# Kernel optimization log

Measured on AMD Instinct MI355X. Metric: run time of the kernel, lower is better.

## Reference

```python
import jax, jax.numpy as jnp
import numpy as np

T, B, H = 400, 256, 256
XE, SE, NX, NS = 32, 16, 100, 5
DIN = XE + H + 1  # x_emb + f_old(hidden) + treatment scalar


def _gru(x, h, wih, whh, bih, bhh):
    # torch.nn.GRUCell math, gate order r,z,n
    gx = x @ wih + bih
    gh = h @ whh + bhh
    xr, xz, xn = jnp.split(gx, 3, axis=-1)
    hr, hz, hn = jnp.split(gh, 3, axis=-1)
    r = jax.nn.sigmoid(xr + hr)
    z = jax.nn.sigmoid(xz + hz)
    n = jnp.tanh(xn + r * hn)
    return (1.0 - z) * n + z * h


def setup_inputs():
    key = jax.random.key(0)
    ks = iter(jax.random.split(key, 64))
    rn = lambda shape, s=0.05: jax.random.normal(next(ks), shape, jnp.float32) * s
    z = lambda n: jnp.zeros((n,), jnp.float32)
    return {
        "x": rn((B, T, NX), 1.0),
        "x_demo": rn((B, NS), 1.0),
        "x_fr": (jax.random.uniform(next(ks), (B, T)) < 0.1).astype(jnp.float32),
        "f_hx0": rn((B, H), 1.0),
        "cf_hx0": rn((B, H), 1.0),
        "w_x2emb": rn((NX, XE)), "b_x2emb": z(XE),
        "w_static": rn((NS, SE)), "b_static": z(SE),
        "wih_f": rn((DIN, 3 * H)), "whh_f": rn((H, 3 * H)), "bih_f": z(3 * H), "bhh_f": z(3 * H),
        "wih_cf": rn((DIN, 3 * H)), "whh_cf": rn((H, 3 * H)), "bih_cf": z(3 * H), "bhh_cf": z(3 * H),
        "w_cat_f": rn((2 * H, H)), "b_cat_f": z(H),
        "w_cat_cf": rn((2 * H, H)), "b_cat_cf": z(H),
        "w_ipw": rn((XE + H + SE, H)), "b_ipw": z(H), "w_ipw_out": rn((H, 1)),
        "w_of": rn((XE + H + SE + 1, H)), "b_of": z(H), "w_ho_f": rn((H, 1)),
        "w_ocf": rn((XE + H + SE + 1, H)), "b_ocf": z(H), "w_ho_cf": rn((H, 1)),
    }


def _forward(x, x_demo, x_fr, f_hx0, cf_hx0,
             w_x2emb, b_x2emb, w_static, b_static,
             wih_f, whh_f, bih_f, bhh_f,
             wih_cf, whh_cf, bih_cf, bhh_cf,
             w_cat_f, b_cat_f, w_cat_cf, b_cat_cf,
             w_ipw, b_ipw, w_ipw_out,
             w_of, b_of, w_ho_f,
             w_ocf, b_ocf, w_ho_cf):
    x_emb_all = jnp.einsum('btf,fe->tbe', x, w_x2emb) + b_x2emb  # (T,B,XE)
    cf_tr = (x_fr.sum(1) == 0).astype(x.dtype)[:, None]          # (B,1), constant over steps
    tidx = jnp.arange(T)

    def attn_ctx(h, buf, i):
        # 'dot' attention of current hidden vs previous hiddens (positions < i)
        scores = jnp.sum(h[None, :, :] * buf, axis=-1)            # (T,B)
        scores = jnp.where((tidx < i)[:, None], scores, -1e30)
        w = jax.nn.softmax(scores, axis=0)
        return jnp.einsum('tb,tbh->bh', w, buf)                   # (B,H)

    def step(carry, xs):
        i, f_hx, cf_hx, f_old, cf_old, f_buf, cf_buf = carry
        x_emb, fr_t = xs
        f_zx = jnp.concatenate([x_emb, f_old], -1)                # (B,XE+H)
        cf_zx = jnp.concatenate([x_emb, cf_old], -1)
        f_hx = _gru(jnp.concatenate([f_zx, fr_t[:, None]], -1), f_hx, wih_f, whh_f, bih_f, bhh_f)
        cf_hx = _gru(jnp.concatenate([cf_zx, cf_tr], -1), cf_hx, wih_cf, whh_cf, bih_cf, bhh_cf)
        # i == 0: torch concatenates (f_hx, f_hx); otherwise attention context
        f_ctx = jnp.where(i == 0, f_hx, attn_ctx(f_hx, f_buf, i))
        cf_ctx = jnp.where(i == 0, cf_hx, attn_ctx(cf_hx, cf_buf, i))
        f_old = jnp.tanh(jnp.concatenate([f_hx, f_ctx], -1) @ w_cat_f + b_cat_f)
        cf_old = jnp.tanh(jnp.concatenate([cf_hx, cf_ctx], -1) @ w_cat_cf + b_cat_cf)
        f_buf = f_buf.at[i].set(f_hx)
        cf_buf = cf_buf.at[i].set(cf_hx)
        return (i + 1, f_hx, cf_hx, f_old, cf_old, f_buf, cf_buf), (f_zx, cf_zx)

    init = (jnp.int32(0), f_hx0, cf_hx0, f_hx0, cf_hx0,
            jnp.zeros((T, B, H), x.dtype), jnp.zeros((T, B, H), x.dtype))
    _, (f_zxs, cf_zxs) = jax.lax.scan(step, init, (x_emb_all, x_fr.T))  # (T,B,XE+H)

    demo = x_demo @ w_static + b_static                            # (B,SE)
    demo_b = jnp.broadcast_to(demo, (T, B, SE))
    ipw = jax.nn.relu(jnp.concatenate([f_zxs, demo_b], -1) @ w_ipw + b_ipw) @ w_ipw_out  # (T,B,1)
    f_tr = (x_fr.sum(1) > 0).astype(x.dtype)[:, None]
    f_h = jax.nn.relu(jnp.concatenate([f_zxs.max(0), demo, f_tr], -1) @ w_of + b_of)
    f_out = f_h @ w_ho_f
    cf_h = jax.nn.relu(jnp.concatenate([cf_zxs.max(0), demo, 1.0 - f_tr], -1) @ w_ocf + b_ocf)
    cf_out = cf_h @ w_ho_cf
    return ipw, f_out, cf_out, f_h


def reference(x, x_demo, x_fr, f_hx0, cf_hx0,
              w_x2emb, b_x2emb, w_static, b_static,
              wih_f, whh_f, bih_f, bhh_f,
              wih_cf, whh_cf, bih_cf, bhh_cf,
              w_cat_f, b_cat_f, w_cat_cf, b_cat_cf,
              w_ipw, b_ipw, w_ipw_out,
              w_of, b_of, w_ho_f,
              w_ocf, b_ocf, w_ho_cf):
    return _forward(x, x_demo, x_fr, f_hx0, cf_hx0,
                    w_x2emb, b_x2emb, w_static, b_static,
                    wih_f, whh_f, bih_f, bhh_f,
                    wih_cf, whh_cf, bih_cf, bhh_cf,
                    w_cat_f, b_cat_f, w_cat_cf, b_cat_cf,
                    w_ipw, b_ipw, w_ipw_out,
                    w_of, b_of, w_ho_f,
                    w_ocf, b_ocf, w_ho_cf)
```

## Files before the change

### kernel.cpp

```cpp
#include <hip/hip_runtime.h>


#define TT 400
#define BB 256
#define HH 256
#define XEc 32
#define NXc 100
#define SEc 16
#define G3 768
#define KXc 289

constexpr size_t XEMB_O     = 0;
constexpr size_t FBUF_O     = XEMB_O     + (size_t)TT*BB*XEc;
constexpr size_t CFBUF_O    = FBUF_O     + (size_t)BB*TT*HH;
constexpr size_t FHX_O      = CFBUF_O    + (size_t)BB*TT*HH;
constexpr size_t CFHX_O     = FHX_O      + (size_t)2*BB*HH;
constexpr size_t FOLD_O     = CFHX_O     + (size_t)2*BB*HH;
constexpr size_t CFOLD_O    = FOLD_O     + (size_t)2*BB*HH;
constexpr size_t CTXF_O     = CFOLD_O    + (size_t)2*BB*HH;
constexpr size_t CTXCF_O    = CTXF_O     + (size_t)BB*HH;
constexpr size_t DEMO_O     = CTXCF_O    + (size_t)BB*HH;
constexpr size_t DEMOIPW_O  = DEMO_O     + (size_t)BB*SEc;
constexpr size_t TRF_O      = DEMOIPW_O  + (size_t)BB*HH;
constexpr size_t XEMBMAX_O  = TRF_O      + (size_t)BB;
constexpr size_t FOLDMAX_O  = XEMBMAX_O  + (size_t)BB*XEc;
constexpr size_t CFOLDMAX_O = FOLDMAX_O  + (size_t)BB*HH;
constexpr size_t BAR_O      = CFOLDMAX_O + (size_t)BB*HH;
constexpr int    BAR_WORDS  = 4096;

constexpr size_t IPW_OUT   = 0;
constexpr size_t FOUT_OUT  = 102400;
constexpr size_t CFOUT_OUT = 102656;
constexpr size_t FH_OUT    = 102912;

struct P {
  const float *x, *x_demo, *x_fr, *f_hx0, *cf_hx0;
  const float *w_x2emb, *b_x2emb, *w_static, *b_static;
  const float *wih_f, *whh_f, *bih_f, *bhh_f;
  const float *wih_cf, *whh_cf, *bih_cf, *bhh_cf;
  const float *w_cat_f, *b_cat_f, *w_cat_cf, *b_cat_cf;
  const float *w_ipw, *b_ipw, *w_ipw_out;
  const float *w_of, *b_of, *w_ho_f;
  const float *w_ocf, *b_ocf, *w_ho_cf;
  float *out; float *ws;
};

__device__ __forceinline__ float sigm(float v) { return 1.f / (1.f + expf(-v)); }

__device__ __forceinline__ void gsyncg(float* ws, int wg, unsigned target) {
  __syncthreads();
  unsigned* flags = reinterpret_cast<unsigned*>(ws + BAR_O);
  const int tid = threadIdx.x;
  if (tid == 0)
    __hip_atomic_store(&flags[wg * 16], target, __ATOMIC_RELEASE, __HIP_MEMORY_SCOPE_AGENT);
  const int gbase = (wg & ~15) * 16;
  if (tid < 16) {
    while (__hip_atomic_load(&flags[gbase + tid * 16], __ATOMIC_ACQUIRE,
                             __HIP_MEMORY_SCOPE_AGENT) < target)
      __builtin_amdgcn_s_sleep(1);
  }
  __syncthreads();
}

__global__ __launch_bounds__(256) void preA_k(P p) {
  __shared__ float wle[NXc * XEc];
  __shared__ float xt[64 * NXc];
  float* ws = p.ws;
  const int t = blockIdx.x;
  for (int i = threadIdx.x; i < NXc * XEc; i += 256) wle[i] = p.w_x2emb[i];
  const int e = threadIdx.x & 31, r0 = threadIdx.x >> 5;
  for (int bt = 0; bt < 4; ++bt) {
    __syncthreads();
    for (int i = threadIdx.x; i < 64 * NXc; i += 256) {
      int r = i / NXc, f = i - r * NXc;
      xt[i] = p.x[((size_t)(bt * 64 + r) * TT + t) * NXc + f];
    }
    __syncthreads();
    for (int r = r0; r < 64; r += 8) {
      const float* xr = xt + r * NXc;
      float acc = p.b_x2emb[e];
      for (int f = 0; f < NXc; ++f) acc += xr[f] * wle[f * XEc + e];
      ws[XEMB_O + ((size_t)t * BB + bt * 64 + r) * XEc + e] = acc;
    }
  }
}

__global__ __launch_bounds__(256) void preB_k(P p) {
  float* ws = p.ws;
  const int tid = threadIdx.x;
  const int blk = blockIdx.x;
  if (blk < 32) {
    int g = blk * 256 + tid;
    int b = g >> 5, e = g & 31;
    float m = -3.4e38f;
    for (int t = 0; t < TT; ++t)
      m = fmaxf(m, ws[XEMB_O + ((size_t)t * BB + b) * XEc + e]);
    ws[XEMBMAX_O + g] = m;
  } else if (blk < 64) {
    int g = (blk - 32) * 256 + tid;
    for (size_t i = g; i < 102912; i += 8192) p.out[i] = 0.f;
  } else if (blk == 64) {
    for (int i = tid; i < BB * SEc; i += 256) {
      int b = i >> 4, se = i & 15;
      float acc = p.b_static[se];
      for (int ns = 0; ns < 5; ++ns) acc += p.x_demo[b * 5 + ns] * p.w_static[ns * SEc + se];
      ws[DEMO_O + i] = acc;
    }
  } else if (blk < 81) {
    int g = (blk - 65) * 256 + tid;
    for (int i = g; i < BB * HH; i += 4096) {
      int b = i >> 8, j = i & 255;
      float acc = 0.f;
      for (int se = 0; se < SEc; ++se) {
        float d = p.b_static[se];
        for (int ns = 0; ns < 5; ++ns) d += p.x_demo[b * 5 + ns] * p.w_static[ns * SEc + se];
        acc += d * p.w_ipw[(size_t)(288 + se) * HH + j];
      }
      ws[DEMOIPW_O + i] = acc;
    }
  } else if (blk == 81) {
    int b = tid;
    float s = 0.f;
    for (int t = 0; t < TT; ++t) s += p.x_fr[(size_t)b * TT + t];
    ws[TRF_O + b] = (s > 0.f) ? 1.f : 0.f;
  } else if (blk < 98) {
    int g = (blk - 82) * 256 + tid;
    for (int i = g; i < 6 * BB * HH; i += 4096) {
      int a = i >> 16, r = i & 65535;
      float vf = p.f_hx0[r], vc = p.cf_hx0[r];
      size_t off; float v;
      switch (a) {
        case 0: off = FHX_O;      v = vf; break;
        case 1: off = CFHX_O;     v = vc; break;
        case 2: off = FOLD_O;     v = vf; break;
        case 3: off = CFOLD_O;    v = vc; break;
        case 4: off = FOLDMAX_O;  v = vf; break;
        default: off = CFOLDMAX_O; v = vc; break;
      }
      ws[off + r] = v;
    }
  } else if (blk == 98) {
    unsigned* bw = reinterpret_cast<unsigned*>(ws + BAR_O);
    for (int i = tid; i < BAR_WORDS; i += 256) bw[i] = 0u;
  }
}

__global__ __launch_bounds__(1024) void seq_k(P p) {
  __shared__ float lds[13344];
  float* ws = p.ws;
  const int tid = threadIdx.x;
  const int wg = blockIdx.x;
  const int btile = wg >> 4, slice = wg & 15;
  const int cell = slice >> 3, sl = slice & 7;
  const int b0 = btile * 16;
  const int khalf = tid >> 9;
  const int gr = (tid & 511) >> 5;
  const int gc = tid & 31;
  const int jo = sl * 32 + gc;

  unsigned tgt = 1;

  for (int t = 0; t < TT; ++t) {
    const int rd = t & 1, wr = 1 - rd;

    {
      float* ax  = lds;
      float* ah  = lds + 4640;
      float* red = lds + 8752;
      const float* oldv = ws + (cell ? CFOLD_O : FOLD_O) + (size_t)rd * BB * HH;
      const float* hxv  = ws + (cell ? CFHX_O  : FHX_O ) + (size_t)rd * BB * HH;
      float*       hxn  = ws + (cell ? CFHX_O  : FHX_O ) + (size_t)wr * BB * HH;

      for (int i = tid; i < 16 * KXc; i += 1024) {
        int r = i / KXc, k = i - r * KXc; int b = b0 + r; float v;
        if (k < XEc)            v = ws[XEMB_O + ((size_t)t * BB + b) * XEc + k];
        else if (k < XEc + HH)  v = oldv[(size_t)b * HH + (k - XEc)];
        else                    v = cell ? (1.0f - ws[TRF_O + b]) : p.x_fr[(size_t)b * TT + t];
        ax[r * 290 + k] = v;
      }
      for (int i = tid; i < 16 * 256; i += 1024) {
        int r = i >> 8, k = i & 255;
        ah[r * 257 + k] = hxv[(size_t)(b0 + r) * HH + k];
      }
      __syncthreads();

      float g0 = 0.f, g1 = 0.f, g2 = 0.f;
      if (khalf == 0) {
        const float* a  = ax + gr * 290;
        const float* wk = (cell ? p.wih_cf : p.wih_f) + jo;
        #pragma unroll 4
        for (int k = 0; k < KXc; ++k) {
          float av = a[k];
          g0 += av * wk[0]; g1 += av * wk[256]; g2 += av * wk[512];
          wk += G3;
        }
      } else {
        const float* a  = ah + gr * 257;
        const float* wk = (cell ? p.whh_cf : p.whh_f) + jo;
        #pragma unroll 4
        for (int k = 0; k < 256; ++k) {
          float av = a[k];
          g0 += av * wk[0]; g1 += av * wk[256]; g2 += av * wk[512];
          wk += G3;
        }
      }
      if (khalf == 1) {
        float* rp = red + (gr * 32 + gc) * 3;
        rp[0] = g0; rp[1] = g1; rp[2] = g2;
      }
      __syncthreads();
      if (khalf == 0) {
        const float* bih = cell ? p.bih_cf : p.bih_f;
        const float* bhh = cell ? p.bhh_cf : p.bhh_f;
        const float* rp = red + (gr * 32 + gc) * 3;
        float hr = rp[0], hz = rp[1], hn = rp[2];
        float hprev = ah[gr * 257 + jo];
        float r0 = sigm(g0 + bih[jo]       + hr + bhh[jo]);
        float z0 = sigm(g1 + bih[jo + 256] + hz + bhh[jo + 256]);
        float n0 = tanhf(g2 + bih[jo + 512] + r0 * (hn + bhh[jo + 512]));
        hxn[(size_t)(b0 + gr) * HH + jo] = (1.f - z0) * n0 + z0 * hprev;
      }
    }
    gsyncg(ws, wg, tgt++);

    {
      const int b = wg;
      for (int c = 0; c < 2; ++c) {
        const float* hnew = ws + (c ? CFHX_O : FHX_O) + (size_t)wr * BB * HH + (size_t)b * HH;
        float* buf = ws + (c ? CFBUF_O : FBUF_O) + (size_t)b * TT * HH;
        float* ctx = ws + (c ? CTXCF_O : CTXF_O) + (size_t)b * HH;
        float* q = lds;
        if (tid < 256) { float v = hnew[tid]; q[tid] = v; buf[(size_t)t * HH + tid] = v; }
        __syncthreads();
        if (t == 0) {
          if (tid < 256) ctx[tid] = q[tid];
          __syncthreads();
        } else {
          const int wv = tid >> 6, ln = tid & 63;
          float q0 = q[ln], q1 = q[ln + 64], q2 = q[ln + 128], q3 = q[ln + 192];
          float m = -1e30f, ssum = 0.f, c0 = 0.f, c1 = 0.f, c2 = 0.f, c3 = 0.f;
          int tp = wv;
          for (; tp + 16 < t; tp += 32) {
            const float* ka = buf + (size_t)tp * HH;
            const float* kb = buf + (size_t)(tp + 16) * HH;
            float a0 = ka[ln], a1 = ka[ln + 64], a2 = ka[ln + 128], a3 = ka[ln + 192];
            float e0 = kb[ln], e1 = kb[ln + 64], e2 = kb[ln + 128], e3 = kb[ln + 192];
            float da = a0 * q0 + a1 * q1 + a2 * q2 + a3 * q3;
            float db = e0 * q0 + e1 * q1 + e2 * q2 + e3 * q3;
            #pragma unroll
            for (int off = 32; off; off >>= 1) {
              da += __shfl_xor(da, off, 64);
              db += __shfl_xor(db, off, 64);
            }
            float nm = fmaxf(m, fmaxf(da, db));
            float al = expf(m - nm), pa = expf(da - nm), pb = expf(db - nm);
            ssum = ssum * al + pa + pb;
            c0 = c0 * al + pa * a0 + pb * e0;
            c1 = c1 * al + pa * a1 + pb * e1;
            c2 = c2 * al + pa * a2 + pb * e2;
            c3 = c3 * al + pa * a3 + pb * e3;
            m = nm;
          }
          if (tp < t) {
            const float* kr = buf + (size_t)tp * HH;
            float a0 = kr[ln], a1 = kr[ln + 64], a2 = kr[ln + 128], a3 = kr[ln + 192];
            float d = a0 * q0 + a1 * q1 + a2 * q2 + a3 * q3;
            #pragma unroll
            for (int off = 32; off; off >>= 1) d += __shfl_xor(d, off, 64);
            float nm = fmaxf(m, d);
            float al = expf(m - nm), pv = expf(d - nm);
            ssum = ssum * al + pv;
            c0 = c0 * al + pv * a0; c1 = c1 * al + pv * a1;
            c2 = c2 * al + pv * a2; c3 = c3 * al + pv * a3;
            m = nm;
          }
          float* cm = lds + 256; float* cs = lds + 272; float* cc = lds + 288;
          if (ln == 0) { cm[wv] = m; cs[wv] = ssum; }
          cc[wv * 256 + ln]       = c0;
          cc[wv * 256 + ln + 64]  = c1;
          cc[wv * 256 + ln + 128] = c2;
          cc[wv * 256 + ln + 192] = c3;
          __syncthreads();
          if (tid < 256) {
            float M = cm[0];
            #pragma unroll
            for (int w2 = 1; w2 < 16; ++w2) M = fmaxf(M, cm[w2]);
            float S = 0.f, num = 0.f;
            #pragma unroll
            for (int w2 = 0; w2 < 16; ++w2) {
              float e = expf(cm[w2] - M);
              S   += cs[w2] * e;
              num += cc[w2 * 256 + tid] * e;
            }
            ctx[tid] = num / S;
          }
          __syncthreads();
        }
      }
    }
    gsyncg(ws, wg, tgt++);

    {
      float* ct   = lds;
      float* it   = lds + 8208;
      float* red2 = lds + 12832;
      const float* hnew = ws + (cell ? CFHX_O : FHX_O) + (size_t)wr * BB * HH;
      const float* ctxv = ws + (cell ? CTXCF_O : CTXF_O);
      for (int i = tid; i < 16 * 512; i += 1024) {
        int r = i >> 9, k = i & 511; int b = b0 + r;
        ct[r * 513 + k] = (k < 256) ? hnew[(size_t)b * HH + k]
                                    : ctxv[(size_t)b * HH + (k - 256)];
      }
      for (int i = tid; i < 16 * 288; i += 1024) {
        int r = i / 288, k = i - r * 288; int b = b0 + r;
        it[r * 289 + k] = (k < 32) ? ws[XEMB_O + ((size_t)t * BB + b) * XEc + k]
                                   : ws[FOLD_O + (size_t)rd * BB * HH + (size_t)b * HH + (k - 32)];
      }
      __syncthreads();

      {
        const float* wc = cell ? p.w_cat_cf : p.w_cat_f;
        float a0 = 0.f;
        const float* ar = ct + gr * 513 + khalf * 256;
        const float* wp = wc + (size_t)(khalf * 256) * HH + jo;
        #pragma unroll 4
        for (int k = 0; k < 256; ++k) { a0 += ar[k] * wp[0]; wp += HH; }
        if (khalf == 1) red2[gr * 32 + gc] = a0;
        __syncthreads();
        if (khalf == 0) {
          const float* bc = cell ? p.b_cat_cf : p.b_cat_f;
          float f0 = tanhf(a0 + red2[gr * 32 + gc] + bc[jo]);
          int b = b0 + gr;
          float* on = ws + (cell ? CFOLD_O : FOLD_O) + (size_t)wr * BB * HH;
          on[(size_t)b * HH + jo] = f0;
          if (t < TT - 1) {
            float* fm = ws + (cell ? CFOLDMAX_O : FOLDMAX_O);
            fm[(size_t)b * HH + jo] = fmaxf(fm[(size_t)b * HH + jo], f0);
          }
        }
      }
      {
        const int ir = tid >> 6, il = tid & 63;
        const int itj = il >> 2, ikq = il & 3;
        const int cI = slice * 16 + itj;
        const int b = b0 + ir;
        float acc = 0.f;
        const float* itr = it + ir * 289;
        const float* wi = p.w_ipw + cI;
        #pragma unroll 4
        for (int k = ikq * 72; k < ikq * 72 + 72; ++k) acc += itr[k] * wi[(size_t)k * HH];
        acc += __shfl_xor(acc, 1, 64);
        acc += __shfl_xor(acc, 2, 64);
        float tot = acc + p.b_ipw[cI] + ws[DEMOIPW_O + (size_t)b * HH + cI];
        float pr = (tot > 0.f) ? tot * p.w_ipw_out[cI] : 0.f;
        pr += __shfl_xor(pr, 4, 64);
        pr += __shfl_xor(pr, 8, 64);
        pr += __shfl_xor(pr, 16, 64);
        pr += __shfl_xor(pr, 32, 64);
        if (il == 0) atomicAdd(p.out + IPW_OUT + (size_t)t * BB + b, pr);
      }
    }
    gsyncg(ws, wg, tgt++);
  }
}

__global__ __launch_bounds__(256) void post_k(P p) {
  __shared__ float at[16 * 306];
  float* ws = p.ws;
  const int tid = threadIdx.x;
  const int wg = blockIdx.x;
  const int btile = wg >> 4, slice = wg & 15;
  const int cell = slice >> 3, sl = slice & 7;
  const int b0 = btile * 16;
  const int tb = tid >> 4, tj = tid & 15;

  for (int i = tid; i < 16 * 305; i += 256) {
    int r = i / 305, k = i - r * 305; int b = b0 + r; float v;
    if (k < 32)        v = ws[XEMBMAX_O + (size_t)b * XEc + k];
    else if (k < 288)  v = ws[(cell ? CFOLDMAX_O : FOLDMAX_O) + (size_t)b * HH + (k - 32)];
    else if (k < 304)  v = ws[DEMO_O + (size_t)b * SEc + (k - 288)];
    else { float tr = ws[TRF_O + b]; v = cell ? (1.f - tr) : tr; }
    at[r * 306 + k] = v;
  }
  __syncthreads();

  const int jo = sl * 32 + tj * 2;
  const float* wo  = cell ? p.w_ocf   : p.w_of;
  const float* bo  = cell ? p.b_ocf   : p.b_of;
  const float* who = cell ? p.w_ho_cf : p.w_ho_f;
  float a0 = 0.f, a1 = 0.f;
  const float* ar = at + tb * 306;
  const float* wop = wo + jo;
  for (int k = 0; k < 305; ++k) {
    float a = ar[k];
    float2 w = *(const float2*)(wop + (size_t)k * HH);
    a0 += a * w.x; a1 += a * w.y;
  }
  int b = b0 + tb;
  float h0 = fmaxf(a0 + bo[jo], 0.f), h1 = fmaxf(a1 + bo[jo + 1], 0.f);
  if (!cell) {
    p.out[FH_OUT + (size_t)b * HH + jo]     = h0;
    p.out[FH_OUT + (size_t)b * HH + jo + 1] = h1;
  }
  float pr = h0 * who[jo] + h1 * who[jo + 1];
  pr += __shfl_xor(pr, 8, 16);
  pr += __shfl_xor(pr, 4, 16);
  pr += __shfl_xor(pr, 2, 16);
  pr += __shfl_xor(pr, 1, 16);
  if (tj == 0) atomicAdd(p.out + (cell ? CFOUT_OUT : FOUT_OUT) + b, pr);
}

extern "C" void kernel_launch(void* const* d_in, const int* in_sizes, int n_in,
                              void* d_out, int out_size, void* d_ws, size_t ws_size,
                              hipStream_t stream) {
  (void)in_sizes; (void)n_in; (void)out_size; (void)ws_size;
  P p;
  p.x        = (const float*)d_in[0];
  p.x_demo   = (const float*)d_in[1];
  p.x_fr     = (const float*)d_in[2];
  p.f_hx0    = (const float*)d_in[3];
  p.cf_hx0   = (const float*)d_in[4];
  p.w_x2emb  = (const float*)d_in[5];
  p.b_x2emb  = (const float*)d_in[6];
  p.w_static = (const float*)d_in[7];
  p.b_static = (const float*)d_in[8];
  p.wih_f    = (const float*)d_in[9];
  p.whh_f    = (const float*)d_in[10];
  p.bih_f    = (const float*)d_in[11];
  p.bhh_f    = (const float*)d_in[12];
  p.wih_cf   = (const float*)d_in[13];
  p.whh_cf   = (const float*)d_in[14];
  p.bih_cf   = (const float*)d_in[15];
  p.bhh_cf   = (const float*)d_in[16];
  p.w_cat_f  = (const float*)d_in[17];
  p.b_cat_f  = (const float*)d_in[18];
  p.w_cat_cf = (const float*)d_in[19];
  p.b_cat_cf = (const float*)d_in[20];
  p.w_ipw    = (const float*)d_in[21];
  p.b_ipw    = (const float*)d_in[22];
  p.w_ipw_out= (const float*)d_in[23];
  p.w_of     = (const float*)d_in[24];
  p.b_of     = (const float*)d_in[25];
  p.w_ho_f   = (const float*)d_in[26];
  p.w_ocf    = (const float*)d_in[27];
  p.b_ocf    = (const float*)d_in[28];
  p.w_ho_cf  = (const float*)d_in[29];
  p.out = (float*)d_out;
  p.ws  = (float*)d_ws;

  preA_k<<<dim3(TT), dim3(256), 0, stream>>>(p);
  preB_k<<<dim3(256), dim3(256), 0, stream>>>(p);

  void* kp[] = { &p };
  hipLaunchCooperativeKernel((const void*)seq_k, dim3(256), dim3(1024), kp, 0, stream);

  post_k<<<dim3(256), dim3(256), 0, stream>>>(p);
}
```

Before: 45.92 ms.

## Relax grid-barrier ordering, split GEMV K four ways with paired columns, vectorize attention

The global barrier now uses relaxed agent-scope atomics instead of release/acquire, and polls with a longer sleep. To compensate, every cross-workgroup read and write of shared state goes through relaxed atomic loads and stores. The GRU and cat GEMVs move from a two-way K split with one column per thread to a four-way K split with two adjacent columns per thread. This lets weight loads use float2 and adds a three-way LDS reduction. The attention pass reads keys and the query as float4. The intent is to cut cache-invalidation and barrier overhead and to raise memory-load efficiency. The risks are memory-ordering correctness, since no fences remain, and added wake-up latency from the longer sleep.

Result: slower. 54.69 ms (+19.1%).

```diff
diff --git a/kernel.cpp b/kernel.cpp
--- a/kernel.cpp
+++ b/kernel.cpp
@@ -9,6 +9,9 @@
 #define SEc 16
 #define G3 768
 #define KXc 289
+
+#define AGT __HIP_MEMORY_SCOPE_AGENT
+#define RLX __ATOMIC_RELAXED
 
 constexpr size_t XEMB_O     = 0;
 constexpr size_t FBUF_O     = XEMB_O     + (size_t)TT*BB*XEc;
@@ -47,17 +50,23 @@
 
 __device__ __forceinline__ float sigm(float v) { return 1.f / (1.f + expf(-v)); }
 
+__device__ __forceinline__ float ald(const float* a) {
+  return __hip_atomic_load(a, RLX, AGT);
+}
+__device__ __forceinline__ void ast(float* a, float v) {
+  __hip_atomic_store(a, v, RLX, AGT);
+}
+
 __device__ __forceinline__ void gsyncg(float* ws, int wg, unsigned target) {
   __syncthreads();
   unsigned* flags = reinterpret_cast<unsigned*>(ws + BAR_O);
   const int tid = threadIdx.x;
   if (tid == 0)
-    __hip_atomic_store(&flags[wg * 16], target, __ATOMIC_RELEASE, __HIP_MEMORY_SCOPE_AGENT);
+    __hip_atomic_store(&flags[wg * 16], target, RLX, AGT);
   const int gbase = (wg & ~15) * 16;
   if (tid < 16) {
-    while (__hip_atomic_load(&flags[gbase + tid * 16], __ATOMIC_ACQUIRE,
-                             __HIP_MEMORY_SCOPE_AGENT) < target)
-      __builtin_amdgcn_s_sleep(1);
+    while (__hip_atomic_load(&flags[gbase + tid * 16], RLX, AGT) < target)
+      __builtin_amdgcn_s_sleep(8);
   }
   __syncthreads();
 }
@@ -146,17 +155,17 @@
 }
 
 __global__ __launch_bounds__(1024) void seq_k(P p) {
-  __shared__ float lds[13344];
+  __shared__ float lds[14368];
   float* ws = p.ws;
   const int tid = threadIdx.x;
   const int wg = blockIdx.x;
   const int btile = wg >> 4, slice = wg & 15;
   const int cell = slice >> 3, sl = slice & 7;
   const int b0 = btile * 16;
-  const int khalf = tid >> 9;
-  const int gr = (tid & 511) >> 5;
-  const int gc = tid & 31;
-  const int jo = sl * 32 + gc;
+  const int gcp = tid & 15;
+  const int gr  = (tid >> 4) & 15;
+  const int kq  = tid >> 8;
+  const int jo  = sl * 32 + gcp * 2;
 
   unsigned tgt = 1;
 
@@ -174,51 +183,80 @@
       for (int i = tid; i < 16 * KXc; i += 1024) {
         int r = i / KXc, k = i - r * KXc; int b = b0 + r; float v;
         if (k < XEc)            v = ws[XEMB_O + ((size_t)t * BB + b) * XEc + k];
-        else if (k < XEc + HH)  v = oldv[(size_t)b * HH + (k - XEc)];
+        else if (k < XEc + HH)  v = ald(&oldv[(size_t)b * HH + (k - XEc)]);
         else                    v = cell ? (1.0f - ws[TRF_O + b]) : p.x_fr[(size_t)b * TT + t];
         ax[r * 290 + k] = v;
       }
       for (int i = tid; i < 16 * 256; i += 1024) {
         int r = i >> 8, k = i & 255;
-        ah[r * 257 + k] = hxv[(size_t)(b0 + r) * HH + k];
+        ah[r * 257 + k] = ald(&hxv[(size_t)(b0 + r) * HH + k]);
       }
       __syncthreads();
 
-      float g0 = 0.f, g1 = 0.f, g2 = 0.f;
-      if (khalf == 0) {
+      float g0=0,g1=0,g2=0,g3=0,g4=0,g5=0;
+      if (kq < 2) {
+        const int kbeg = (kq & 1) ? 145 : 0, kend = (kq & 1) ? 289 : 145;
         const float* a  = ax + gr * 290;
-        const float* wk = (cell ? p.wih_cf : p.wih_f) + jo;
-        #pragma unroll 4
-        for (int k = 0; k < KXc; ++k) {
+        const float* wk = (cell ? p.wih_cf : p.wih_f) + (size_t)kbeg * G3 + jo;
+        #pragma unroll 8
+        for (int k = kbeg; k < kend; ++k) {
           float av = a[k];
-          g0 += av * wk[0]; g1 += av * wk[256]; g2 += av * wk[512];
+          float2 w0 = *(const float2*)(wk);
+          float2 w1 = *(const float2*)(wk + 256);
+          float2 w2 = *(const float2*)(wk + 512);
+          g0 += av*w0.x; g1 += av*w0.y;
+          g2 += av*w1.x; g3 += av*w1.y;
+          g4 += av*w2.x; g5 += av*w2.y;
           wk += G3;
         }
       } else {
+        const int kbeg = (kq & 1) ? 128 : 0, kend = kbeg + 128;
         const float* a  = ah + gr * 257;
-        const float* wk = (cell ? p.whh_cf : p.whh_f) + jo;
-        #pragma unroll 4
-        for (int k = 0; k < 256; ++k) {
+        const float* wk = (cell ? p.whh_cf : p.whh_f) + (size_t)kbeg * G3 + jo;
+        #pragma unroll 8
+        for (int k = kbeg; k < kend; ++k) {
           float av = a[k];
-          g0 += av * wk[0]; g1 += av * wk[256]; g2 += av * wk[512];
+          float2 w0 = *(const float2*)(wk);
+          float2 w1 = *(const float2*)(wk + 256);
+          float2 w2 = *(const float2*)(wk + 512);
+          g0 += av*w0.x; g1 += av*w0.y;
+          g2 += av*w1.x; g3 += av*w1.y;
+          g4 += av*w2.x; g5 += av*w2.y;
           wk += G3;
         }
       }
-      if (khalf == 1) {
-        float* rp = red + (gr * 32 + gc) * 3;
-        rp[0] = g0; rp[1] = g1; rp[2] = g2;
+      if (kq != 0) {
+        float* rp = red + (size_t)(kq - 1) * 1536 + (gr * 16 + gcp) * 6;
+        rp[0]=g0; rp[1]=g1; rp[2]=g2; rp[3]=g3; rp[4]=g4; rp[5]=g5;
       }
       __syncthreads();
-      if (khalf == 0) {
+      if (kq == 0) {
         const float* bih = cell ? p.bih_cf : p.bih_f;
         const float* bhh = cell ? p.bhh_cf : p.bhh_f;
-        const float* rp = red + (gr * 32 + gc) * 3;
-        float hr = rp[0], hz = rp[1], hn = rp[2];
-        float hprev = ah[gr * 257 + jo];
-        float r0 = sigm(g0 + bih[jo]       + hr + bhh[jo]);
-        float z0 = sigm(g1 + bih[jo + 256] + hz + bhh[jo + 256]);
-        float n0 = tanhf(g2 + bih[jo + 512] + r0 * (hn + bhh[jo + 512]));
-        hxn[(size_t)(b0 + gr) * HH + jo] = (1.f - z0) * n0 + z0 * hprev;
+        const float* r1 = red +        (gr * 16 + gcp) * 6;
+        const float* r2 = red + 1536 + (gr * 16 + gcp) * 6;
+        const float* r3 = red + 3072 + (gr * 16 + gcp) * 6;
+        int b = b0 + gr;
+        {
+          int j = jo;
+          float xr = g0 + r1[0], xz = g2 + r1[2], xn = g4 + r1[4];
+          float hr = r2[0] + r3[0], hz = r2[2] + r3[2], hn = r2[4] + r3[4];
+          float hprev = ah[gr * 257 + j];
+          float rr = sigm(xr + bih[j]       + hr + bhh[j]);
+          float zz = sigm(xz + bih[j + 256] + hz + bhh[j + 256]);
+          float nn = tanhf(xn + bih[j + 512] + rr * (hn + bhh[j + 512]));
+          ast(&hxn[(size_t)b * HH + j], (1.f - zz) * nn + zz * hprev);
+        }
+        {
+          int j = jo + 1;
+          float xr = g1 + r1[1], xz = g3 + r1[3], xn = g5 + r1[5];
+          float hr = r2[1] + r3[1], hz = r2[3] + r3[3], hn = r2[5] + r3[5];
+          float hprev = ah[gr * 257 + j];
+          float rr = sigm(xr + bih[j]       + hr + bhh[j]);
+          float zz = sigm(xz + bih[j + 256] + hz + bhh[j + 256]);
+          float nn = tanhf(xn + bih[j + 512] + rr * (hn + bhh[j + 512]));
+          ast(&hxn[(size_t)b * HH + j], (1.f - zz) * nn + zz * hprev);
+        }
       }
     }
     gsyncg(ws, wg, tgt++);
@@ -230,23 +268,25 @@
         float* buf = ws + (c ? CFBUF_O : FBUF_O) + (size_t)b * TT * HH;
         float* ctx = ws + (c ? CTXCF_O : CTXF_O) + (size_t)b * HH;
         float* q = lds;
-        if (tid < 256) { float v = hnew[tid]; q[tid] = v; buf[(size_t)t * HH + tid] = v; }
+        if (tid < 256) {
+          float v = ald(&hnew[tid]);
+          q[tid] = v;
+          buf[(size_t)t * HH + tid] = v;
+        }
         __syncthreads();
         if (t == 0) {
-          if (tid < 256) ctx[tid] = q[tid];
+          if (tid < 256) ast(&ctx[tid], q[tid]);
           __syncthreads();
         } else {
           const int wv = tid >> 6, ln = tid & 63;
-          float q0 = q[ln], q1 = q[ln + 64], q2 = q[ln + 128], q3 = q[ln + 192];
+          const float4 qv = *(const float4*)&q[4 * ln];
           float m = -1e30f, ssum = 0.f, c0 = 0.f, c1 = 0.f, c2 = 0.f, c3 = 0.f;
           int tp = wv;
           for (; tp + 16 < t; tp += 32) {
-            const float* ka = buf + (size_t)tp * HH;
-            const float* kb = buf + (size_t)(tp + 16) * HH;
-            float a0 = ka[ln], a1 = ka[ln + 64], a2 = ka[ln + 128], a3 = ka[ln + 192];
-            float e0 = kb[ln], e1 = kb[ln + 64], e2 = kb[ln + 128], e3 = kb[ln + 192];
-            float da = a0 * q0 + a1 * q1 + a2 * q2 + a3 * q3;
-            float db = e0 * q0 + e1 * q1 + e2 * q2 + e3 * q3;
+            const float4 a = *(const float4*)(buf + (size_t)tp * HH + 4 * ln);
+            const float4 e = *(const float4*)(buf + (size_t)(tp + 16) * HH + 4 * ln);
+            float da = a.x*qv.x + a.y*qv.y + a.z*qv.z + a.w*qv.w;
+            float db = e.x*qv.x + e.y*qv.y + e.z*qv.z + e.w*qv.w;
             #pragma unroll
             for (int off = 32; off; off >>= 1) {
               da += __shfl_xor(da, off, 64);
@@ -255,31 +295,27 @@
             float nm = fmaxf(m, fmaxf(da, db));
             float al = expf(m - nm), pa = expf(da - nm), pb = expf(db - nm);
             ssum = ssum * al + pa + pb;
-            c0 = c0 * al + pa * a0 + pb * e0;
-            c1 = c1 * al + pa * a1 + pb * e1;
-            c2 = c2 * al + pa * a2 + pb * e2;
-            c3 = c3 * al + pa * a3 + pb * e3;
+            c0 = c0 * al + pa * a.x + pb * e.x;
+            c1 = c1 * al + pa * a.y + pb * e.y;
+            c2 = c2 * al + pa * a.z + pb * e.z;
+            c3 = c3 * al + pa * a.w + pb * e.w;
             m = nm;
           }
           if (tp < t) {
-            const float* kr = buf + (size_t)tp * HH;
-            float a0 = kr[ln], a1 = kr[ln + 64], a2 = kr[ln + 128], a3 = kr[ln + 192];
-            float d = a0 * q0 + a1 * q1 + a2 * q2 + a3 * q3;
+            const float4 a = *(const float4*)(buf + (size_t)tp * HH + 4 * ln);
+            float d = a.x*qv.x + a.y*qv.y + a.z*qv.z + a.w*qv.w;
             #pragma unroll
             for (int off = 32; off; off >>= 1) d += __shfl_xor(d, off, 64);
             float nm = fmaxf(m, d);
             float al = expf(m - nm), pv = expf(d - nm);
             ssum = ssum * al + pv;
-            c0 = c0 * al + pv * a0; c1 = c1 * al + pv * a1;
-            c2 = c2 * al + pv * a2; c3 = c3 * al + pv * a3;
+            c0 = c0 * al + pv * a.x; c1 = c1 * al + pv * a.y;
+            c2 = c2 * al + pv * a.z; c3 = c3 * al + pv * a.w;
             m = nm;
           }
           float* cm = lds + 256; float* cs = lds + 272; float* cc = lds + 288;
           if (ln == 0) { cm[wv] = m; cs[wv] = ssum; }
-          cc[wv * 256 + ln]       = c0;
-          cc[wv * 256 + ln + 64]  = c1;
-          cc[wv * 256 + ln + 128] = c2;
-          cc[wv * 256 + ln + 192] = c3;
+          *(float4*)&cc[wv * 256 + 4 * ln] = make_float4(c0, c1, c2, c3);
           __syncthreads();
           if (tid < 256) {
             float M = cm[0];
@@ -292,7 +328,7 @@
               S   += cs[w2] * e;
               num += cc[w2 * 256 + tid] * e;
             }
-            ctx[tid] = num / S;
+            ast(&ctx[tid], num / S);
           }
           __syncthreads();
         }
@@ -306,36 +342,51 @@
       float* red2 = lds + 12832;
       const float* hnew = ws + (cell ? CFHX_O : FHX_O) + (size_t)wr * BB * HH;
       const float* ctxv = ws + (cell ? CTXCF_O : CTXF_O);
+      const float* oldr = ws + FOLD_O + (size_t)rd * BB * HH;
       for (int i = tid; i < 16 * 512; i += 1024) {
         int r = i >> 9, k = i & 511; int b = b0 + r;
-        ct[r * 513 + k] = (k < 256) ? hnew[(size_t)b * HH + k]
-                                    : ctxv[(size_t)b * HH + (k - 256)];
+        ct[r * 513 + k] = (k < 256) ? ald(&hnew[(size_t)b * HH + k])
+                                    : ald(&ctxv[(size_t)b * HH + (k - 256)]);
       }
       for (int i = tid; i < 16 * 288; i += 1024) {
         int r = i / 288, k = i - r * 288; int b = b0 + r;
         it[r * 289 + k] = (k < 32) ? ws[XEMB_O + ((size_t)t * BB + b) * XEc + k]
-                                   : ws[FOLD_O + (size_t)rd * BB * HH + (size_t)b * HH + (k - 32)];
+                                   : ald(&oldr[(size_t)b * HH + (k - 32)]);
       }
       __syncthreads();
 
       {
         const float* wc = cell ? p.w_cat_cf : p.w_cat_f;
-        float a0 = 0.f;
-        const float* ar = ct + gr * 513 + khalf * 256;
-        const float* wp = wc + (size_t)(khalf * 256) * HH + jo;
-        #pragma unroll 4
-        for (int k = 0; k < 256; ++k) { a0 += ar[k] * wp[0]; wp += HH; }
-        if (khalf == 1) red2[gr * 32 + gc] = a0;
+        float a0 = 0.f, a1 = 0.f;
+        const float* ar = ct + gr * 513 + kq * 128;
+        const float* wp = wc + (size_t)(kq * 128) * HH + jo;
+        #pragma unroll 8
+        for (int k = 0; k < 128; ++k) {
+          float av = ar[k];
+          float2 w = *(const float2*)(wp);
+          a0 += av * w.x; a1 += av * w.y;
+          wp += HH;
+        }
+        if (kq != 0) {
+          float* rp = red2 + (kq - 1) * 512 + (gr * 16 + gcp) * 2;
+          rp[0] = a0; rp[1] = a1;
+        }
         __syncthreads();
-        if (khalf == 0) {
+        if (kq == 0) {
           const float* bc = cell ? p.b_cat_cf : p.b_cat_f;
-          float f0 = tanhf(a0 + red2[gr * 32 + gc] + bc[jo]);
+          const float* r1 = red2 +        (gr * 16 + gcp) * 2;
+          const float* r2 = red2 + 512  + (gr * 16 + gcp) * 2;
+          const float* r3 = red2 + 1024 + (gr * 16 + gcp) * 2;
           int b = b0 + gr;
+          float f0 = tanhf(a0 + r1[0] + r2[0] + r3[0] + bc[jo]);
+          float f1 = tanhf(a1 + r1[1] + r2[1] + r3[1] + bc[jo + 1]);
           float* on = ws + (cell ? CFOLD_O : FOLD_O) + (size_t)wr * BB * HH;
-          on[(size_t)b * HH + jo] = f0;
+          ast(&on[(size_t)b * HH + jo],     f0);
+          ast(&on[(size_t)b * HH + jo + 1], f1);
           if (t < TT - 1) {
             float* fm = ws + (cell ? CFOLDMAX_O : FOLDMAX_O);
-            fm[(size_t)b * HH + jo] = fmaxf(fm[(size_t)b * HH + jo], f0);
+            fm[(size_t)b * HH + jo]     = fmaxf(fm[(size_t)b * HH + jo], f0);
+            fm[(size_t)b * HH + jo + 1] = fmaxf(fm[(size_t)b * HH + jo + 1], f1);
           }
         }
       }
```
